# Kernel optimization log

Hardware: AMD Instinct MI355X
Metric: run time of the kernel (lower is better)

## Reference

```python
import jax, jax.numpy as jnp
import numpy as np
from jax.scipy.special import digamma

ALPHA_DP = 1e-3  # alphaDP from __init__
LOG2 = float(np.log(2.0))


def setup_inputs() -> dict:
    key = jax.random.key(0)
    k1, k2 = jax.random.split(key)
    N, D, T = 1_500_000, 4, 16
    data = jax.random.normal(k1, (N, D), dtype=jnp.float32)
    Phi = jax.random.uniform(k2, (N, T), dtype=jnp.float32)
    Phi = Phi / jnp.sum(Phi, axis=1, keepdims=True)  # soft responsibilities (original uses one-hot multinomial)
    priorMu = jnp.ones((D, 1), dtype=jnp.float32)          # priorGaussianMeanMu
    priorKappa = 0.1 * jnp.ones((1,), dtype=jnp.float32)    # priorGaussianVarKappa
    priorPsi = jnp.eye(D, dtype=jnp.float32)                # priorWishartPsi
    priorNu = 200.0 * jnp.ones((1,), dtype=jnp.float32)     # priorWishartNu
    return {"data": data, "Phi": Phi, "priorMu": priorMu, "priorKappa": priorKappa,
            "priorPsi": priorPsi, "priorNu": priorNu}


def reference(data, Phi, priorMu, priorKappa, priorPsi, priorNu):
    # One VB-EM iteration: vbMStep followed by vbEStep, returning updated Phi.
    N, D = data.shape
    T = Phi.shape[1]

    # ---------------- M-step ----------------
    Nk = jnp.sum(Phi, axis=0)                      # [T] soft counts
    g1 = 1.0 + Nk                                  # BetaGamma1
    # BetaGamma2[a] = alpha + sum_{b>a} Nk[b] (stick-breaking tail mass; replaces the [T,N,T] mask)
    tail = jnp.cumsum(Nk[::-1])[::-1]              # sum_{b>=a} Nk[b]
    g2 = ALPHA_DP + (tail - Nk)

    prior11 = priorPsi + priorKappa * (priorMu @ priorMu.T)     # [D,D]
    # S[t] = sum_n Phi[n,t] * x_n x_n^T  (vectorizes the per-cluster bmm loop)
    S = jnp.einsum('ni,nd,ne->ide', Phi, data, data)            # [T,D,D]
    T12 = priorKappa * priorMu + data.T @ Phi                   # [D,T]
    kappa = priorKappa + Nk                                     # [T] variationalGaussianVarKappa
    mu = T12 / kappa[None, :]                                   # [D,T] variationalGaussianMeanMu
    nu = Nk + priorNu                                           # [T] variationalWishartNu
    # Psi_t = prior11 + S_t - kappa_t * mu_t mu_t^T  (== -2*T11 - kappa*mu mu^T)
    Psi = prior11[None, :, :] + S - kappa[:, None, None] * jnp.einsum('dt,et->tde', mu, mu)  # [T,D,D]

    # ---------------- E-step ----------------
    dg_sum = digamma(g1 + g2)
    dg1 = digamma(g1) - dg_sum                     # [T] E[log v_t]
    dg2 = digamma(g2) - dg_sum                     # [T] E[log(1-v_t)]
    term2 = jnp.cumsum(dg2) - dg2                  # exclusive prefix sum_{a<t} dg2[a]

    Psi_inv = jnp.linalg.inv(Psi)                  # [T,D,D]
    Lam = nu[:, None, None] * Psi_inv              # [T,D,D] E[Lambda_t]
    eta2 = jnp.einsum('tde,et->td', Lam, mu)       # [T,D] Lambda_t mu_t
    eta3 = -digamma(0.5 * nu) - D * LOG2 + jnp.log(jnp.linalg.det(Psi))   # [T]
    quad = jnp.einsum('dt,tde,et->t', mu, Psi_inv, mu)                    # mu_t^T Psi_t^{-1} mu_t
    eta4 = -0.5 * D / kappa - 0.5 * nu * quad      # [T]

    term31 = -0.5 * jnp.einsum('nd,tde,ne->nt', data, Lam, data)
    term32 = data @ eta2.T                                                # [N,T]

    logits = (dg1 + term2 - 0.5 * eta3 + eta4)[None, :] + term31 + term32 # [N,T]
    # original: exp then row-normalize == softmax
    Phi_new = jax.nn.softmax(logits, axis=-1)
    return Phi_new
```

## Files before the change

kernel.cpp:

```cpp
#include <hip/hip_runtime.h>
#include <math.h>

#define TT 16
#define DD 4
#define NB1 2048

__device__ double digammad(double x) {
    double r = 0.0;
    while (x < 6.0) { r -= 1.0 / x; x += 1.0; }
    double xi = 1.0 / x;
    double xi2 = xi * xi;
    double s = log(x) - 0.5 * xi
        - xi2 * (1.0 / 12.0 - xi2 * (1.0 / 120.0 - xi2 * (1.0 / 252.0
            - xi2 * (1.0 / 240.0 - xi2 * (1.0 / 132.0)))));
    return r + s;
}

__global__ __launch_bounds__(256) void k1_reduce(
        const float* __restrict__ data, const float* __restrict__ Phi,
        float* __restrict__ partials, int N) {
    const int tid = threadIdx.x;
    const int lane = tid & 63;
    const int wave = tid >> 6;
    const int t = tid & 15;
    const int s = tid >> 4;

    float acc[15];
    #pragma unroll
    for (int k = 0; k < 15; ++k) acc[k] = 0.f;

    const int stride = 64 * gridDim.x;
    for (int pbase = blockIdx.x * 64; pbase < N; pbase += stride) {
        int q[4]; float ph[4]; float4 xv[4];
        #pragma unroll
        for (int u = 0; u < 4; ++u) {
            int qq = pbase + s + 16 * u;
            int qc = qq < N ? qq : N - 1;
            q[u] = qq;
            xv[u] = *reinterpret_cast<const float4*>(data + (size_t)qc * 4);
            ph[u] = Phi[(size_t)qc * 16 + t];
        }
        #pragma unroll
        for (int u = 0; u < 4; ++u) {
            float f = q[u] < N ? ph[u] : 0.f;
            float4 x = xv[u];
            float fx = f * x.x, fy = f * x.y, fz = f * x.z, fw = f * x.w;
            acc[0] += f;
            acc[1] += fx; acc[2] += fy; acc[3] += fz; acc[4] += fw;
            acc[5] += fx * x.x; acc[6]  += fx * x.y; acc[7]  += fx * x.z; acc[8] += fx * x.w;
            acc[9] += fy * x.y; acc[10] += fy * x.z; acc[11] += fy * x.w;
            acc[12] += fz * x.z; acc[13] += fz * x.w;
            acc[14] += fw * x.w;
        }
    }

    #pragma unroll
    for (int off = 16; off < 64; off <<= 1)
        #pragma unroll
        for (int k = 0; k < 15; ++k)
            acc[k] += __shfl_xor(acc[k], off, 64);

    __shared__ float lds[4 * 240];
    if (lane < 16) {
        #pragma unroll
        for (int k = 0; k < 15; ++k)
            lds[wave * 240 + t * 15 + k] = acc[k];
    }
    __syncthreads();
    if (tid < 240) {
        partials[(size_t)blockIdx.x * 240 + tid] =
            lds[tid] + lds[240 + tid] + lds[480 + tid] + lds[720 + tid];
    }
}

__global__ __launch_bounds__(256) void k1b_sum(
        const float* __restrict__ partials, double* __restrict__ sums, int nb) {
    const int v = blockIdx.x;
    const int tid = threadIdx.x;
    double a = 0.0;
    for (int b = tid; b < nb; b += 256)
        a += (double)partials[(size_t)b * 240 + v];
    #pragma unroll
    for (int off = 1; off < 64; off <<= 1)
        a += __shfl_xor(a, off, 64);
    __shared__ double w[4];
    if ((tid & 63) == 0) w[tid >> 6] = a;
    __syncthreads();
    if (tid == 0) sums[v] = (w[0] + w[1]) + (w[2] + w[3]);
}

__global__ __launch_bounds__(64) void k2_finalize(
        const double* __restrict__ sums_g,
        const float* __restrict__ priorMu, const float* __restrict__ priorKappa,
        const float* __restrict__ priorPsi, const float* __restrict__ priorNu,
        float* __restrict__ coef) {
    __shared__ double sums[240];
    __shared__ double nk_s[TT], dg2_s[TT], dg1_s[TT];
    const int tid = threadIdx.x;

    if (tid < 60) {
        #pragma unroll
        for (int r = 0; r < 4; ++r) sums[r * 60 + tid] = sums_g[r * 60 + tid];
    }
    __syncthreads();
    if (tid < TT) nk_s[tid] = sums[tid * 15 + 0];
    __syncthreads();

    if (tid < TT) {
        int t = tid;
        double Nk = nk_s[t];
        double tailExcl = 0.0;
        for (int b = t + 1; b < TT; ++b) tailExcl += nk_s[b];
        double g1 = 1.0 + Nk;
        double g2 = 1e-3 + tailExcl;
        double dgs = digammad(g1 + g2);
        dg1_s[t] = digammad(g1) - dgs;
        dg2_s[t] = digammad(g2) - dgs;
    }
    __syncthreads();

    if (tid < TT) {
        const int t = tid;
        const double LOG2 = 0.6931471805599453;
        double term2 = 0.0;
        for (int a = 0; a < t; ++a) term2 += dg2_s[a];
        double Nk = nk_s[t];
        double k0 = (double)priorKappa[0];
        double nu0 = (double)priorNu[0];
        double kappa = k0 + Nk;
        double nu = Nk + nu0;
        double mu[4];
        #pragma unroll
        for (int d = 0; d < 4; ++d)
            mu[d] = (k0 * (double)priorMu[d] + sums[t * 15 + 1 + d]) / kappa;

        const int sidx[4][4] = {{0,1,2,3},{1,4,5,6},{2,5,7,8},{3,6,8,9}};
        double Psi[4][4];
        #pragma unroll
        for (int d = 0; d < 4; ++d)
            #pragma unroll
            for (int e = 0; e < 4; ++e) {
                double pr = (double)priorPsi[d * 4 + e]
                          + k0 * (double)priorMu[d] * (double)priorMu[e];
                Psi[d][e] = pr + sums[t * 15 + 5 + sidx[d][e]] - kappa * mu[d] * mu[e];
            }

        double L00 = sqrt(Psi[0][0]);
        double L10 = Psi[1][0] / L00, L20 = Psi[2][0] / L00, L30 = Psi[3][0] / L00;
        double L11 = sqrt(Psi[1][1] - L10 * L10);
        double L21 = (Psi[2][1] - L20 * L10) / L11;
        double L31 = (Psi[3][1] - L30 * L10) / L11;
        double L22 = sqrt(Psi[2][2] - L20 * L20 - L21 * L21);
        double L32 = (Psi[3][2] - L30 * L20 - L31 * L21) / L22;
        double L33 = sqrt(Psi[3][3] - L30 * L30 - L31 * L31 - L32 * L32);
        double logdet = 2.0 * (log(L00) + log(L11) + log(L22) + log(L33));
        double i00 = 1.0 / L00, i11 = 1.0 / L11, i22 = 1.0 / L22, i33 = 1.0 / L33;
        double i10 = -L10 * i00 * i11;
        double i21 = -L21 * i11 * i22;
        double i32 = -L32 * i22 * i33;
        double i20 = -(L20 * i00 + L21 * i10) * i22;
        double i31 = -(L31 * i11 + L32 * i21) * i33;
        double i30 = -(L30 * i00 + L31 * i10 + L32 * i20) * i33;
        double P00 = i00*i00 + i10*i10 + i20*i20 + i30*i30;
        double P01 = i10*i11 + i20*i21 + i30*i31;
        double P02 = i20*i22 + i30*i32;
        double P03 = i30*i33;
        double P11 = i11*i11 + i21*i21 + i31*i31;
        double P12 = i21*i22 + i31*i32;
        double P13 = i31*i33;
        double P22 = i22*i22 + i32*i32;
        double P23 = i32*i33;
        double P33 = i33*i33;

        double quad = P00*mu[0]*mu[0] + P11*mu[1]*mu[1] + P22*mu[2]*mu[2] + P33*mu[3]*mu[3]
            + 2.0 * (P01*mu[0]*mu[1] + P02*mu[0]*mu[2] + P03*mu[0]*mu[3]
                   + P12*mu[1]*mu[2] + P13*mu[1]*mu[3] + P23*mu[2]*mu[3]);
        double e2_0 = nu * (P00*mu[0] + P01*mu[1] + P02*mu[2] + P03*mu[3]);
        double e2_1 = nu * (P01*mu[0] + P11*mu[1] + P12*mu[2] + P13*mu[3]);
        double e2_2 = nu * (P02*mu[0] + P12*mu[1] + P22*mu[2] + P23*mu[3]);
        double e2_3 = nu * (P03*mu[0] + P13*mu[1] + P23*mu[2] + P33*mu[3]);
        double eta3 = -digammad(0.5 * nu) - 4.0 * LOG2 + logdet;
        double eta4 = -0.5 * 4.0 / kappa - 0.5 * nu * quad;
        double c = dg1_s[t] + term2 - 0.5 * eta3 + eta4;

        float* cf = coef + t * 16;
        cf[0] = (float)c;
        cf[1] = (float)e2_0; cf[2] = (float)e2_1; cf[3] = (float)e2_2; cf[4] = (float)e2_3;
        cf[5]  = (float)(-0.5 * nu * P00);
        cf[6]  = (float)(-nu * P01);
        cf[7]  = (float)(-nu * P02);
        cf[8]  = (float)(-nu * P03);
        cf[9]  = (float)(-0.5 * nu * P11);
        cf[10] = (float)(-nu * P12);
        cf[11] = (float)(-nu * P13);
        cf[12] = (float)(-0.5 * nu * P22);
        cf[13] = (float)(-nu * P23);
        cf[14] = (float)(-0.5 * nu * P33);
        cf[15] = 0.f;
    }
}

__global__ __launch_bounds__(256) void k3_estep(
        const float* __restrict__ data, const float* __restrict__ coef,
        float* __restrict__ out, int N) {
    const int tg = threadIdx.x & 3;
    const int pg = threadIdx.x >> 2;

    float c0[4], ce[4][4], cm[4][10];
    #pragma unroll
    for (int j = 0; j < 4; ++j) {
        const float* c = coef + (tg * 4 + j) * 16;
        c0[j] = c[0];
        #pragma unroll
        for (int d = 0; d < 4; ++d) ce[j][d] = c[1 + d];
        #pragma unroll
        for (int k = 0; k < 10; ++k) cm[j][k] = c[5 + k];
    }

    const int stride = (blockDim.x >> 2) * gridDim.x;
    for (int p = blockIdx.x * (blockDim.x >> 2) + pg; p < N; p += stride) {
        float4 x = *reinterpret_cast<const float4*>(data + (size_t)p * 4);
        float xx[10];
        xx[0] = x.x * x.x; xx[1] = x.x * x.y; xx[2] = x.x * x.z; xx[3] = x.x * x.w;
        xx[4] = x.y * x.y; xx[5] = x.y * x.z; xx[6] = x.y * x.w;
        xx[7] = x.z * x.z; xx[8] = x.z * x.w; xx[9] = x.w * x.w;
        float lg[4];
        #pragma unroll
        for (int j = 0; j < 4; ++j) {
            float v = c0[j];
            v += ce[j][0] * x.x + ce[j][1] * x.y + ce[j][2] * x.z + ce[j][3] * x.w;
            #pragma unroll
            for (int k = 0; k < 10; ++k) v += cm[j][k] * xx[k];
            lg[j] = v;
        }
        float mx = fmaxf(fmaxf(lg[0], lg[1]), fmaxf(lg[2], lg[3]));
        mx = fmaxf(mx, __shfl_xor(mx, 1, 64));
        mx = fmaxf(mx, __shfl_xor(mx, 2, 64));
        float e0 = __expf(lg[0] - mx), e1 = __expf(lg[1] - mx);
        float e2 = __expf(lg[2] - mx), e3 = __expf(lg[3] - mx);
        float s = (e0 + e1) + (e2 + e3);
        s += __shfl_xor(s, 1, 64);
        s += __shfl_xor(s, 2, 64);
        float r = 1.0f / s;
        float4 o = make_float4(e0 * r, e1 * r, e2 * r, e3 * r);
        *reinterpret_cast<float4*>(out + (size_t)p * 16 + tg * 4) = o;
    }
}

extern "C" void kernel_launch(void* const* d_in, const int* in_sizes, int n_in,
                              void* d_out, int out_size, void* d_ws, size_t ws_size,
                              hipStream_t stream) {
    const float* data = (const float*)d_in[0];
    const float* Phi = (const float*)d_in[1];
    const float* priorMu = (const float*)d_in[2];
    const float* priorKappa = (const float*)d_in[3];
    const float* priorPsi = (const float*)d_in[4];
    const float* priorNu = (const float*)d_in[5];
    float* out = (float*)d_out;
    const int N = in_sizes[0] / DD;

    int nb = NB1;
    for (;;) {
        size_t off_sums = (((size_t)nb * 240 * 4) + 7) & ~(size_t)7;
        size_t need = off_sums + 240 * 8 + 256 * 4;
        if (need <= ws_size || nb <= 1) break;
        nb >>= 1;
    }
    size_t off_sums = (((size_t)nb * 240 * 4) + 7) & ~(size_t)7;

    float* partials = (float*)d_ws;
    double* sums = (double*)((char*)d_ws + off_sums);
    float* coef = (float*)((char*)d_ws + off_sums + 240 * 8);

    k1_reduce<<<nb, 256, 0, stream>>>(data, Phi, partials, N);
    k1b_sum<<<240, 256, 0, stream>>>(partials, sums, nb);
    k2_finalize<<<1, 64, 0, stream>>>(sums, priorMu, priorKappa, priorPsi,
                                      priorNu, coef);
    k3_estep<<<2048, 256, 0, stream>>>(data, coef, out, N);
}
```

Measured before the change: 75.82 us.

## Stage Phi tiles through LDS with coalesced float4 loads in reduction kernel

Result: slower. 89.23 us (+17.7%).

```diff
diff --git a/kernel.cpp b/kernel.cpp
--- a/kernel.cpp
+++ b/kernel.cpp
@@ -3,7 +3,7 @@
 
 #define TT 16
 #define DD 4
-#define NB1 2048
+#define PHI_LD 260
 
 __device__ double digammad(double x) {
     double r = 0.0;
@@ -19,6 +19,7 @@
 __global__ __launch_bounds__(256) void k1_reduce(
         const float* __restrict__ data, const float* __restrict__ Phi,
         float* __restrict__ partials, int N) {
+    __shared__ float lds[16 * PHI_LD];
     const int tid = threadIdx.x;
     const int lane = tid & 63;
     const int wave = tid >> 6;
@@ -29,29 +30,44 @@
     #pragma unroll
     for (int k = 0; k < 15; ++k) acc[k] = 0.f;
 
-    const int stride = 64 * gridDim.x;
-    for (int pbase = blockIdx.x * 64; pbase < N; pbase += stride) {
-        int q[4]; float ph[4]; float4 xv[4];
-        #pragma unroll
-        for (int u = 0; u < 4; ++u) {
-            int qq = pbase + s + 16 * u;
-            int qc = qq < N ? qq : N - 1;
-            q[u] = qq;
-            xv[u] = *reinterpret_cast<const float4*>(data + (size_t)qc * 4);
-            ph[u] = Phi[(size_t)qc * 16 + t];
+    const int stride = 256 * gridDim.x;
+    for (int base = blockIdx.x * 256; base < N; base += stride) {
+        #pragma unroll
+        for (int j = 0; j < 4; ++j) {
+            int m = tid + 256 * j;
+            int pm = m >> 2;
+            int cb = (m & 3) * 4;
+            int pg = base + pm;
+            int pc = pg < N ? pg : N - 1;
+            float4 v = *reinterpret_cast<const float4*>(Phi + (size_t)pc * 16 + cb);
+            if (pg >= N) v = make_float4(0.f, 0.f, 0.f, 0.f);
+            lds[(cb + 0) * PHI_LD + pm] = v.x;
+            lds[(cb + 1) * PHI_LD + pm] = v.y;
+            lds[(cb + 2) * PHI_LD + pm] = v.z;
+            lds[(cb + 3) * PHI_LD + pm] = v.w;
         }
-        #pragma unroll
-        for (int u = 0; u < 4; ++u) {
-            float f = q[u] < N ? ph[u] : 0.f;
-            float4 x = xv[u];
-            float fx = f * x.x, fy = f * x.y, fz = f * x.z, fw = f * x.w;
-            acc[0] += f;
-            acc[1] += fx; acc[2] += fy; acc[3] += fz; acc[4] += fw;
-            acc[5] += fx * x.x; acc[6]  += fx * x.y; acc[7]  += fx * x.z; acc[8] += fx * x.w;
-            acc[9] += fy * x.y; acc[10] += fy * x.z; acc[11] += fy * x.w;
-            acc[12] += fz * x.z; acc[13] += fz * x.w;
-            acc[14] += fw * x.w;
+        __syncthreads();
+
+        #pragma unroll
+        for (int g = 0; g < 4; ++g) {
+            float4 pv = *reinterpret_cast<float4*>(&lds[t * PHI_LD + s * 16 + g * 4]);
+            float ph4[4] = {pv.x, pv.y, pv.z, pv.w};
+            #pragma unroll
+            for (int ii = 0; ii < 4; ++ii) {
+                int pg = base + s * 16 + g * 4 + ii;
+                int pc = pg < N ? pg : N - 1;
+                float4 x = *reinterpret_cast<const float4*>(data + (size_t)pc * 4);
+                float f = ph4[ii];
+                float fx = f * x.x, fy = f * x.y, fz = f * x.z, fw = f * x.w;
+                acc[0] += f;
+                acc[1] += fx; acc[2] += fy; acc[3] += fz; acc[4] += fw;
+                acc[5] += fx * x.x; acc[6]  += fx * x.y; acc[7]  += fx * x.z; acc[8] += fx * x.w;
+                acc[9] += fy * x.y; acc[10] += fy * x.z; acc[11] += fy * x.w;
+                acc[12] += fz * x.z; acc[13] += fz * x.w;
+                acc[14] += fw * x.w;
+            }
         }
+        __syncthreads();
     }
 
     #pragma unroll
@@ -60,7 +76,6 @@
         for (int k = 0; k < 15; ++k)
             acc[k] += __shfl_xor(acc[k], off, 64);
 
-    __shared__ float lds[4 * 240];
     if (lane < 16) {
         #pragma unroll
         for (int k = 0; k < 15; ++k)
@@ -259,12 +274,12 @@
     float* out = (float*)d_out;
     const int N = in_sizes[0] / DD;
 
-    int nb = NB1;
+    int nb = (N + 255) / 256;
     for (;;) {
         size_t off_sums = (((size_t)nb * 240 * 4) + 7) & ~(size_t)7;
         size_t need = off_sums + 240 * 8 + 256 * 4;
         if (need <= ws_size || nb <= 1) break;
-        nb >>= 1;
+        nb = (nb + 1) >> 1;
     }
     size_t off_sums = (((size_t)nb * 240 * 4) + 7) & ~(size_t)7;
 
```

## Double-buffer reduction tiles via direct global-to-LDS async loads

Applied to the files above, without the earlier changes.

Measured after the change: 80.65 us. +6.4%, slower.

```diff
diff --git a/kernel.cpp b/kernel.cpp
--- a/kernel.cpp
+++ b/kernel.cpp
@@ -3,7 +3,13 @@
 
 #define TT 16
 #define DD 4
-#define NB1 2048
+#define NB1 1024
+
+__device__ __forceinline__ void gload_lds16(const float* g, float* l) {
+    __builtin_amdgcn_global_load_lds(
+        (const __attribute__((address_space(1))) void*)g,
+        (__attribute__((address_space(3))) void*)l, 16, 0, 0);
+}
 
 __device__ double digammad(double x) {
     double r = 0.0;
@@ -19,31 +25,53 @@
 __global__ __launch_bounds__(256) void k1_reduce(
         const float* __restrict__ data, const float* __restrict__ Phi,
         float* __restrict__ partials, int N) {
+    __shared__ float phi_s[2][4096];
+    __shared__ float x_s[2][1024];
     const int tid = threadIdx.x;
     const int lane = tid & 63;
     const int wave = tid >> 6;
     const int t = tid & 15;
-    const int s = tid >> 4;
+    const int slot = tid >> 4;
+
+    const size_t phiMax = (size_t)N * 16 - 4;
+    const size_t xMax = (size_t)N * 4 - 4;
+    const int ntiles = (N + 255) / 256;
 
     float acc[15];
     #pragma unroll
     for (int k = 0; k < 15; ++k) acc[k] = 0.f;
 
-    const int stride = 64 * gridDim.x;
-    for (int pbase = blockIdx.x * 64; pbase < N; pbase += stride) {
-        int q[4]; float ph[4]; float4 xv[4];
-        #pragma unroll
-        for (int u = 0; u < 4; ++u) {
-            int qq = pbase + s + 16 * u;
-            int qc = qq < N ? qq : N - 1;
-            q[u] = qq;
-            xv[u] = *reinterpret_cast<const float4*>(data + (size_t)qc * 4);
-            ph[u] = Phi[(size_t)qc * 16 + t];
+    auto stage = [&](int tk, int b) {
+        const size_t p0f = (size_t)tk * 256;
+        #pragma unroll
+        for (int j = 0; j < 4; ++j) {
+            int c = wave * 4 + j;
+            size_t gi = p0f * 16 + (size_t)c * 256 + lane * 4;
+            if (gi > phiMax) gi = phiMax;
+            gload_lds16(Phi + gi, &phi_s[b][c * 256]);
         }
-        #pragma unroll
-        for (int u = 0; u < 4; ++u) {
-            float f = q[u] < N ? ph[u] : 0.f;
-            float4 x = xv[u];
+        size_t gx = p0f * 4 + (size_t)wave * 256 + lane * 4;
+        if (gx > xMax) gx = xMax;
+        gload_lds16(data + gx, &x_s[b][wave * 256]);
+    };
+
+    const int t0 = blockIdx.x;
+    if (t0 < ntiles) stage(t0, 0);
+    __syncthreads();
+
+    int k = 0;
+    for (int tk = t0; tk < ntiles; tk += gridDim.x, ++k) {
+        const int cur = k & 1;
+        const int nxt = tk + gridDim.x;
+        if (nxt < ntiles) stage(nxt, 1 - cur);
+
+        const int P0 = tk * 256;
+        #pragma unroll
+        for (int i = 0; i < 16; ++i) {
+            int pl = slot * 16 + ((i + slot) & 15);
+            float f = phi_s[cur][pl * 16 + t];
+            float4 x = *reinterpret_cast<const float4*>(&x_s[cur][pl * 4]);
+            f = (P0 + pl < N) ? f : 0.f;
             float fx = f * x.x, fy = f * x.y, fz = f * x.z, fw = f * x.w;
             acc[0] += f;
             acc[1] += fx; acc[2] += fy; acc[3] += fz; acc[4] += fw;
@@ -52,24 +80,24 @@
             acc[12] += fz * x.z; acc[13] += fz * x.w;
             acc[14] += fw * x.w;
         }
+        __syncthreads();
     }
 
     #pragma unroll
     for (int off = 16; off < 64; off <<= 1)
         #pragma unroll
-        for (int k = 0; k < 15; ++k)
-            acc[k] += __shfl_xor(acc[k], off, 64);
-
-    __shared__ float lds[4 * 240];
+        for (int kk = 0; kk < 15; ++kk)
+            acc[kk] += __shfl_xor(acc[kk], off, 64);
+
     if (lane < 16) {
         #pragma unroll
-        for (int k = 0; k < 15; ++k)
-            lds[wave * 240 + t * 15 + k] = acc[k];
+        for (int kk = 0; kk < 15; ++kk)
+            phi_s[0][wave * 240 + t * 15 + kk] = acc[kk];
     }
     __syncthreads();
     if (tid < 240) {
         partials[(size_t)blockIdx.x * 240 + tid] =
-            lds[tid] + lds[240 + tid] + lds[480 + tid] + lds[720 + tid];
+            phi_s[0][tid] + phi_s[0][240 + tid] + phi_s[0][480 + tid] + phi_s[0][720 + tid];
     }
 }
 
@@ -261,8 +289,8 @@
 
     int nb = NB1;
     for (;;) {
-        size_t off_sums = (((size_t)nb * 240 * 4) + 7) & ~(size_t)7;
-        size_t need = off_sums + 240 * 8 + 256 * 4;
+        size_t off_sums0 = (((size_t)nb * 240 * 4) + 7) & ~(size_t)7;
+        size_t need = off_sums0 + 240 * 8 + 256 * 4;
         if (need <= ws_size || nb <= 1) break;
         nb >>= 1;
     }
```
